# Optimization experiments

Measured on AMD Instinct MI355X. Metric: run time of the kernel, lower is better.

Reference implementation:

```python
import jax, jax.numpy as jnp
import numpy as np

D = 768
H = 12
DH = D // H
EPS = 1e-5

def _ln(x, g, b):
    m = jnp.mean(x, axis=-1, keepdims=True)
    v = jnp.mean(jnp.square(x - m), axis=-1, keepdims=True)
    return (x - m) * jax.lax.rsqrt(v + EPS) * g + b

def _gelu_new(x):
    c = jnp.float32(0.7978845608028654)  # sqrt(2/pi)
    return 0.5 * x * (1.0 + jnp.tanh(c * (x + 0.044715 * x * x * x)))

def setup_inputs() -> dict:
    key = jax.random.key(0)
    ks = jax.random.split(key, 12)
    s = lambda fan: 1.0 / np.sqrt(fan)
    return {
        "x": jax.random.normal(ks[0], (2, 1024, D), jnp.float32),
        "context_seq": jax.random.normal(ks[1], (2, 256, D), jnp.float32),
        "sos_h": jnp.zeros((D,), jnp.float32),
        "ln1_g": jnp.ones((D,), jnp.float32),
        "ln1_b": jnp.zeros((D,), jnp.float32),
        "W_attn": jax.random.normal(ks[2], (D, 3 * D), jnp.float32) * s(D),
        "b_attn": jnp.zeros((3 * D,), jnp.float32),
        "W_ref": jax.random.normal(ks[3], (D, 2 * D), jnp.float32) * s(D),
        "b_ref": jnp.zeros((2 * D,), jnp.float32),
        "W_proj": jax.random.normal(ks[4], (D, D), jnp.float32) * s(D),
        "b_proj": jnp.zeros((D,), jnp.float32),
        "ln2_g": jnp.ones((D,), jnp.float32),
        "ln2_b": jnp.zeros((D,), jnp.float32),
        "W_fc": jax.random.normal(ks[5], (D, 4 * D), jnp.float32) * s(D),
        "b_fc": jnp.zeros((4 * D,), jnp.float32),
        "W_mproj": jax.random.normal(ks[6], (4 * D, D), jnp.float32) * s(4 * D),
        "b_mproj": jnp.zeros((D,), jnp.float32),
    }

def _split_heads(t):  # [B,T,D] -> [B,H,T,dh]
    B, T, _ = t.shape
    return t.reshape(B, T, H, DH).transpose(0, 2, 1, 3)

def reference(x, context_seq, sos_h, ln1_g, ln1_b, W_attn, b_attn, W_ref, b_ref,
              W_proj, b_proj, ln2_g, ln2_b, W_fc, b_fc, W_mproj, b_mproj):
    B, S, _ = x.shape
    Sc = context_seq.shape[1]
    # prepend sos token (history_seq is None, history_seq_len = 0)
    sos = jnp.broadcast_to(sos_h.reshape(1, 1, D), (B, 1, D))
    h = jnp.concatenate([sos, x], axis=1)          # [B, S+1, D]
    hl = _ln(h, ln1_g, ln1_b)
    qkv = hl @ W_attn + b_attn
    q, k, v = jnp.split(qkv, 3, axis=-1)
    ckv = context_seq @ W_ref + b_ref
    kc, vc = jnp.split(ckv, 2, axis=-1)
    K = jnp.concatenate([kc, k], axis=1)            # [B, Sc+S+1, D]
    V = jnp.concatenate([vc, v], axis=1)
    qh, kh, vh = _split_heads(q), _split_heads(K), _split_heads(V)
    nd, ns = S + 1, Sc + S + 1
    w = jnp.einsum('bhqd,bhkd->bhqk', qh, kh) / jnp.float32(np.sqrt(DH))
    # causal bias window: query i attends to key j iff j <= i + Sc
    mask = jnp.arange(ns)[None, :] <= (jnp.arange(nd)[:, None] + Sc)
    w = jnp.where(mask[None, None], w, jnp.float32(-10000.0))
    w = jax.nn.softmax(w, axis=-1)
    a = jnp.einsum('bhqk,bhkd->bhqd', w, vh)        # [B,H,S+1,dh]
    a = a.transpose(0, 2, 1, 3).reshape(B, nd, D)
    a = a @ W_proj + b_proj
    h = h + a
    m = _gelu_new(_ln(h, ln2_g, ln2_b) @ W_fc + b_fc) @ W_mproj + b_mproj
    h = h + m
    return h[:, 1:, :]                               # drop sos position
```

## Files before the change

### kernel.cpp

```cpp
#include <hip/hip_runtime.h>
#include <math.h>

#define D0 768
#define NH 12
#define DHD 64
#define NB 2
#define SQ 1024
#define SCX 256
#define ND 1025
#define NS 1281
#define TT (NB*ND)
#define TP 2176
#define TC (NB*SCX)

typedef __attribute__((ext_vector_type(8))) short bf16x8;
typedef __attribute__((ext_vector_type(4))) float f32x4;

typedef const __attribute__((address_space(1))) unsigned int* gptr_t;
typedef __attribute__((address_space(3))) unsigned int* lptr_t;

__device__ __forceinline__ unsigned short f2bf(float f) {
    union { float f; unsigned u; } v; v.f = f;
    unsigned r = v.u + 0x7FFFu + ((v.u >> 16) & 1u);
    return (unsigned short)(r >> 16);
}

__device__ __forceinline__ float gelu_new(float x) {
    float x3 = x*x*x;
    float u = 0.7978845608028654f*(x + 0.044715f*x3);
    return 0.5f*x*(1.f + tanhf(u));
}

struct PrepArgs {
    const float* x; const float* sos; float* h;
    const float* ctx; unsigned short* ctxb;
    const float* W[5]; unsigned short* Wt[5];
    int K[5], N[5], nblk[5];
};

#define NBH 1538
#define NCVT 192

__global__ __launch_bounds__(256) void k_prep(PrepArgs a) {
    __shared__ float t[32][33];
    const int tid = threadIdx.x;
    int bid = blockIdx.x;
    if (bid < NBH) {
        int idx = bid*256 + tid;
        if (idx < TT*192) {
            int r = idx/192, c4 = idx%192;
            int b = r/ND, tt = r%ND;
            float4 v;
            if (tt == 0) v = ((const float4*)a.sos)[c4];
            else         v = ((const float4*)a.x)[(size_t)(b*SQ + tt - 1)*192 + c4];
            ((float4*)a.h)[(size_t)r*192 + c4] = v;
        }
        return;
    }
    bid -= NBH;
    if (bid < NCVT) {
        int i = bid*256 + tid;
        float4 p = ((const float4*)a.ctx)[i*2];
        float4 q = ((const float4*)a.ctx)[i*2+1];
        uint4 o;
        o.x = (unsigned)f2bf(p.x) | ((unsigned)f2bf(p.y) << 16);
        o.y = (unsigned)f2bf(p.z) | ((unsigned)f2bf(p.w) << 16);
        o.z = (unsigned)f2bf(q.x) | ((unsigned)f2bf(q.y) << 16);
        o.w = (unsigned)f2bf(q.z) | ((unsigned)f2bf(q.w) << 16);
        ((uint4*)a.ctxb)[i] = o;
        return;
    }
    bid -= NCVT;
    #pragma unroll
    for (int wi = 0; wi < 5; ++wi) {
        if (bid < a.nblk[wi]) {
            const float* W = a.W[wi];
            unsigned short* Wt = a.Wt[wi];
            const int K = a.K[wi], N = a.N[wi];
            const int nbx = N >> 5;
            const int n0 = (bid % nbx)*32, k0 = (bid / nbx)*32;
            const int r = tid >> 3, c4 = (tid & 7)*4;
            float4 v = *(const float4*)&W[(size_t)(k0+r)*N + n0 + c4];
            t[r][c4+0]=v.x; t[r][c4+1]=v.y; t[r][c4+2]=v.z; t[r][c4+3]=v.w;
            __syncthreads();
            ushort4 o;
            o.x = f2bf(t[c4+0][r]); o.y = f2bf(t[c4+1][r]);
            o.z = f2bf(t[c4+2][r]); o.w = f2bf(t[c4+3][r]);
            *(ushort4*)&Wt[(size_t)(n0+r)*K + k0 + c4] = o;
            return;
        }
        bid -= a.nblk[wi];
    }
}

__global__ __launch_bounds__(256) void k_ln(const float* __restrict__ in,
                                            const float* __restrict__ add,
                                            const float* __restrict__ g,
                                            const float* __restrict__ beta,
                                            unsigned short* __restrict__ out,
                                            float* __restrict__ resid,
                                            int nvalid) {
    int r = blockIdx.x;
    int tid = threadIdx.x;
    const size_t base = (size_t)r*D0;
    if (r >= nvalid) {
        out[base+tid] = 0; out[base+tid+256] = 0; out[base+tid+512] = 0;
        return;
    }
    float v0 = in[base+tid], v1 = in[base+tid+256], v2 = in[base+tid+512];
    if (add) {
        v0 += add[base+tid]; v1 += add[base+tid+256]; v2 += add[base+tid+512];
        resid[base+tid] = v0; resid[base+tid+256] = v1; resid[base+tid+512] = v2;
    }
    float s = v0+v1+v2;
    float ss = v0*v0 + v1*v1 + v2*v2;
    #pragma unroll
    for (int o = 32; o >= 1; o >>= 1) {
        s  += __shfl_down(s, o);
        ss += __shfl_down(ss, o);
    }
    __shared__ float red[8];
    __shared__ float mv[2];
    int w = tid >> 6;
    if ((tid & 63) == 0) { red[w] = s; red[4+w] = ss; }
    __syncthreads();
    if (tid == 0) {
        float S1 = red[0]+red[1]+red[2]+red[3];
        float S2 = red[4]+red[5]+red[6]+red[7];
        float mean = S1 * (1.f/D0);
        float var  = S2 * (1.f/D0) - mean*mean;
        mv[0] = mean; mv[1] = rsqrtf(var + 1e-5f);
    }
    __syncthreads();
    float mean = mv[0], rstd = mv[1];
    out[base+tid]     = f2bf((v0-mean)*rstd*g[tid]     + beta[tid]);
    out[base+tid+256] = f2bf((v1-mean)*rstd*g[tid+256] + beta[tid+256]);
    out[base+tid+512] = f2bf((v2-mean)*rstd*g[tid+512] + beta[tid+512]);
}

template<int GELU, int OUTBF>
__device__ __forceinline__ void gemm64_body(unsigned short* As, unsigned short* Bs,
                                            const unsigned short* __restrict__ A,
                                            const unsigned short* __restrict__ Bt,
                                            const float* __restrict__ bias,
                                            void* __restrict__ Cv,
                                            int N, int K, int bx, int by) {
    const int tid = threadIdx.x;
    const int w = tid >> 6;
    const int l = tid & 63;
    const int wm = w >> 1, wn = w & 1;
    const int m0 = by * 64, n0 = bx * 64;

    f32x4 acc[2][2] = {};

    for (int k0 = 0; k0 < K; k0 += 64) {
        __syncthreads();
        #pragma unroll
        for (int i = 0; i < 2; ++i) {
            int s = i*256 + tid;
            int row = s >> 3;
            int ch  = (s & 7) ^ (row & 7);
            const unsigned short* ga = A  + (size_t)(m0 + row)*K + k0 + ch*8;
            const unsigned short* gb = Bt + (size_t)(n0 + row)*K + k0 + ch*8;
            lptr_t la = (lptr_t)(As + (i*256 + w*64)*8);
            lptr_t lb = (lptr_t)(Bs + (i*256 + w*64)*8);
            __builtin_amdgcn_global_load_lds((gptr_t)ga, la, 16, 0, 0);
            __builtin_amdgcn_global_load_lds((gptr_t)gb, lb, 16, 0, 0);
        }
        __syncthreads();
        #pragma unroll
        for (int kc = 0; kc < 2; ++kc) {
            const int kchunk = kc*4 + (l >> 4);
            bf16x8 a[2], b[2];
            #pragma unroll
            for (int mi = 0; mi < 2; ++mi) {
                int row = wm*32 + mi*16 + (l & 15);
                a[mi] = *(const bf16x8*)&As[row*64 + ((kchunk ^ (row & 7))*8)];
            }
            #pragma unroll
            for (int ni = 0; ni < 2; ++ni) {
                int row = wn*32 + ni*16 + (l & 15);
                b[ni] = *(const bf16x8*)&Bs[row*64 + ((kchunk ^ (row & 7))*8)];
            }
            #pragma unroll
            for (int mi = 0; mi < 2; ++mi)
                #pragma unroll
                for (int ni = 0; ni < 2; ++ni)
                    acc[mi][ni] = __builtin_amdgcn_mfma_f32_16x16x32_bf16(a[mi], b[ni], acc[mi][ni], 0, 0, 0);
        }
    }

    float* Cf = (float*)Cv;
    unsigned short* Cb = (unsigned short*)Cv;
    const int rbase = m0 + wm*32 + (l >> 4)*4;
    const int cbase = n0 + wn*32 + (l & 15);
    #pragma unroll
    for (int ni = 0; ni < 2; ++ni) {
        int col = cbase + ni*16;
        float bv = bias[col];
        #pragma unroll
        for (int mi = 0; mi < 2; ++mi) {
            #pragma unroll
            for (int r = 0; r < 4; ++r) {
                int row = rbase + mi*16 + r;
                float v = acc[mi][ni][r] + bv;
                if (GELU) v = gelu_new(v);
                if (OUTBF) Cb[(size_t)row*N + col] = f2bf(v);
                else       Cf[(size_t)row*N + col] = v;
            }
        }
    }
}

template<int GELU, int OUTBF>
__global__ __launch_bounds__(256) void k_gemm64(const unsigned short* __restrict__ A,
                                                const unsigned short* __restrict__ Bt,
                                                const float* __restrict__ bias,
                                                void* __restrict__ Cv,
                                                int N, int K) {
    __shared__ unsigned short As[64*64];
    __shared__ unsigned short Bs[64*64];
    gemm64_body<GELU,OUTBF>(As, Bs, A, Bt, bias, Cv, N, K, blockIdx.x, blockIdx.y);
}

__global__ __launch_bounds__(256) void k_gemm_qkvckv(const unsigned short* __restrict__ hlb,
                                                     const unsigned short* __restrict__ WatT,
                                                     const float* __restrict__ bat,
                                                     unsigned short* __restrict__ qkvb,
                                                     const unsigned short* __restrict__ ctxb,
                                                     const unsigned short* __restrict__ WrefT,
                                                     const float* __restrict__ bref,
                                                     unsigned short* __restrict__ ckvb) {
    __shared__ unsigned short As[64*64];
    __shared__ unsigned short Bs[64*64];
    int bid = blockIdx.x;
    if (bid < (2304/64)*(TP/64)) {
        gemm64_body<0,1>(As, Bs, hlb, WatT, bat, qkvb, 2304, 768, bid % (2304/64), bid / (2304/64));
    } else {
        bid -= (2304/64)*(TP/64);
        gemm64_body<0,1>(As, Bs, ctxb, WrefT, bref, ckvb, 1536, 768, bid % (1536/64), bid / (1536/64));
    }
}

__global__ __launch_bounds__(256, 2) void k_attn_mfma(const unsigned short* __restrict__ qkvb,
                                                      const unsigned short* __restrict__ ckvb,
                                                      unsigned short* __restrict__ attnob) {
    const int bh = blockIdx.y;
    const int b = bh / NH, hh = bh % NH;
    const int tid = threadIdx.x;
    const int w = tid >> 6;
    const int l = tid & 63;
    const int lg = l >> 4;
    const int ll = l & 15;

    const int q0 = (16 - blockIdx.x) * 64;
    const int qw = q0 + w*16;

    __shared__ unsigned short Ks[64*64];
    __shared__ unsigned short Vt[64*64];
    __shared__ unsigned short Ps[4][16*64];

    bf16x8 qf[2];
    {
        int qc = min(qw + ll, ND-1);
        const unsigned short* qrow = qkvb + (size_t)(b*ND + qc)*2304 + hh*64;
        qf[0] = *(const bf16x8*)(qrow + lg*8);
        qf[1] = *(const bf16x8*)(qrow + 32 + lg*8);
    }

    f32x4 o_acc[4] = {};
    float mrow[4], lrow[4];
    #pragma unroll
    for (int i = 0; i < 4; ++i) { mrow[i] = -1e30f; lrow[i] = 0.f; }

    const int qmax_blk = min(q0 + 63, ND-1);
    const int ntiles = (qmax_blk + SCX)/64 + 1;
    const int klim_wave = qw + 15 + SCX;

    for (int kt = 0; kt < ntiles; ++kt) {
        __syncthreads();
        #pragma unroll
        for (int it = 0; it < 2; ++it) {
            int slot = it*256 + tid;
            int key  = slot >> 3;
            int ch   = (slot & 7) ^ (key & 7);
            int kg   = min(kt*64 + key, NS-1);
            const unsigned short* src;
            if (kg < SCX) src = ckvb + (size_t)(b*SCX + kg)*1536 + hh*64 + ch*8;
            else          src = qkvb + (size_t)(b*ND + kg - SCX)*2304 + 768 + hh*64 + ch*8;
            __builtin_amdgcn_global_load_lds((gptr_t)src, (lptr_t)(Ks + (size_t)(it*256 + w*64)*8), 16, 0, 0);
        }
        {
            int kv0 = (tid & 31)*2;
            int dch = tid >> 5;
            int kg0 = min(kt*64 + kv0,     NS-1);
            int kg1 = min(kt*64 + kv0 + 1, NS-1);
            const unsigned short* s0 = (kg0 < SCX)
                ? ckvb + (size_t)(b*SCX + kg0)*1536 + 768 + hh*64 + dch*8
                : qkvb + (size_t)(b*ND + kg0 - SCX)*2304 + 1536 + hh*64 + dch*8;
            const unsigned short* s1 = (kg1 < SCX)
                ? ckvb + (size_t)(b*SCX + kg1)*1536 + 768 + hh*64 + dch*8
                : qkvb + (size_t)(b*ND + kg1 - SCX)*2304 + 1536 + hh*64 + dch*8;
            union { uint4 u; unsigned short s[8]; } r0, r1;
            r0.u = *(const uint4*)s0;
            r1.u = *(const uint4*)s1;
            #pragma unroll
            for (int i = 0; i < 8; ++i) {
                int d = dch*8 + i;
                unsigned val = (unsigned)r0.s[i] | ((unsigned)r1.s[i] << 16);
                *(unsigned*)((char*)Vt + d*128 + (((kv0>>3) ^ (d&7))*16) + ((kv0&7)*2)) = val;
            }
        }
        __syncthreads();

        if (kt*64 > klim_wave) continue;

        bf16x8 kf[4][2];
        #pragma unroll
        for (int c = 0; c < 4; ++c) {
            int key = c*16 + ll;
            #pragma unroll
            for (int kc = 0; kc < 2; ++kc)
                kf[c][kc] = *(const bf16x8*)((char*)Ks + key*128 + (((kc*4 + lg) ^ (key&7))*16));
        }
        f32x4 s_acc[4];
        #pragma unroll
        for (int c = 0; c < 4; ++c) {
            f32x4 z = {0.f, 0.f, 0.f, 0.f};
            z = __builtin_amdgcn_mfma_f32_16x16x32_bf16(qf[0], kf[c][0], z, 0, 0, 0);
            s_acc[c] = __builtin_amdgcn_mfma_f32_16x16x32_bf16(qf[1], kf[c][1], z, 0, 0, 0);
        }

        const int kbase = kt*64;
        if (kbase + 63 > qw + SCX) {
            #pragma unroll
            for (int c = 0; c < 4; ++c) {
                int key = kbase + c*16 + ll;
                #pragma unroll
                for (int i = 0; i < 4; ++i) {
                    int q = qw + lg*4 + i;
                    if (key > q + SCX) s_acc[c][i] = -1e30f;
                }
            }
        }

        float tmax[4];
        #pragma unroll
        for (int i = 0; i < 4; ++i) {
            float tm = fmaxf(fmaxf(s_acc[0][i], s_acc[1][i]),
                             fmaxf(s_acc[2][i], s_acc[3][i]));
            #pragma unroll
            for (int o = 1; o < 16; o <<= 1) tm = fmaxf(tm, __shfl_xor(tm, o));
            tmax[i] = tm;
        }
        #pragma unroll
        for (int i = 0; i < 4; ++i) {
            float mnew = fmaxf(mrow[i], tmax[i]*0.125f);
            float fs = __expf(mrow[i] - mnew);
            mrow[i] = mnew;
            lrow[i] *= fs;
            #pragma unroll
            for (int dc = 0; dc < 4; ++dc) o_acc[dc][i] *= fs;
        }
        float psum[4] = {0.f, 0.f, 0.f, 0.f};
        #pragma unroll
        for (int c = 0; c < 4; ++c) {
            int kv = c*16 + ll;
            #pragma unroll
            for (int i = 0; i < 4; ++i) {
                float p = __expf(fmaf(s_acc[c][i], 0.125f, -mrow[i]));
                psum[i] += p;
                int q = lg*4 + i;
                union { float f; unsigned u; } cv; cv.f = p;
                *(unsigned short*)((char*)Ps[w] + q*128 + (((kv>>3) ^ (q&7))*16) + ((kv&7)*2))
                    = (unsigned short)((cv.u + 0x8000u) >> 16);
            }
        }
        #pragma unroll
        for (int i = 0; i < 4; ++i) {
            float s = psum[i];
            #pragma unroll
            for (int o = 1; o < 16; o <<= 1) s += __shfl_xor(s, o);
            lrow[i] += s;
        }

        #pragma unroll
        for (int kc = 0; kc < 2; ++kc) {
            int q = ll;
            bf16x8 pf = *(const bf16x8*)((char*)Ps[w] + q*128 + (((kc*4 + lg) ^ (q&7))*16));
            #pragma unroll
            for (int dc = 0; dc < 4; ++dc) {
                int d = dc*16 + ll;
                bf16x8 vf = *(const bf16x8*)((char*)Vt + d*128 + (((kc*4 + lg) ^ (d&7))*16));
                o_acc[dc] = __builtin_amdgcn_mfma_f32_16x16x32_bf16(pf, vf, o_acc[dc], 0, 0, 0);
            }
        }
    }

    #pragma unroll
    for (int i = 0; i < 4; ++i) {
        int q = qw + lg*4 + i;
        if (q >= ND) continue;
        float inv = 1.f / lrow[i];
        unsigned short* orow = attnob + (size_t)(b*ND + q)*768 + hh*64;
        #pragma unroll
        for (int dc = 0; dc < 4; ++dc)
            orow[dc*16 + ll] = f2bf(o_acc[dc][i] * inv);
    }
}

__global__ void k_final(const float* __restrict__ h, const float* __restrict__ mp,
                        float* __restrict__ out) {
    int idx = blockIdx.x*blockDim.x + threadIdx.x;
    const int total = NB*SQ*192;
    if (idx >= total) return;
    int r = idx/192, c4 = idx%192;
    int b = r/SQ, t = r%SQ;
    size_t hr = (size_t)(b*ND + t + 1)*192 + c4;
    float4 hv = ((const float4*)h)[hr];
    float4 mv = ((const float4*)mp)[hr];
    ((float4*)out)[idx] = make_float4(hv.x+mv.x, hv.y+mv.y, hv.z+mv.z, hv.w+mv.w);
}

extern "C" void kernel_launch(void* const* d_in, const int* in_sizes, int n_in,
                              void* d_out, int out_size, void* d_ws, size_t ws_size,
                              hipStream_t stream) {
    const float* x     = (const float*)d_in[0];
    const float* ctx   = (const float*)d_in[1];
    const float* sos   = (const float*)d_in[2];
    const float* ln1g  = (const float*)d_in[3];
    const float* ln1b  = (const float*)d_in[4];
    const float* Wat   = (const float*)d_in[5];
    const float* bat   = (const float*)d_in[6];
    const float* Wref  = (const float*)d_in[7];
    const float* bref  = (const float*)d_in[8];
    const float* Wpj   = (const float*)d_in[9];
    const float* bpj   = (const float*)d_in[10];
    const float* ln2g  = (const float*)d_in[11];
    const float* ln2b  = (const float*)d_in[12];
    const float* Wfc   = (const float*)d_in[13];
    const float* bfc   = (const float*)d_in[14];
    const float* Wmp   = (const float*)d_in[15];
    const float* bmp   = (const float*)d_in[16];
    float* out = (float*)d_out;

    char* p = (char*)d_ws;
    float* h      = (float*)p;  p += (size_t)TP*768*4;
    float* aproj  = (float*)p;  p += (size_t)TP*768*4;
    unsigned short* qkvb   = (unsigned short*)p;  p += (size_t)TP*2304*2;
    unsigned short* ckvb   = (unsigned short*)p;  p += (size_t)TC*1536*2;
    unsigned short* hlb    = (unsigned short*)p;  p += (size_t)TP*768*2;
    unsigned short* attnob = (unsigned short*)p;  p += (size_t)TP*768*2;
    unsigned short* mfcb   = (unsigned short*)p;  p += (size_t)TP*3072*2;
    unsigned short* ctxb   = (unsigned short*)p;  p += (size_t)TC*768*2;
    unsigned short* WatT   = (unsigned short*)p;  p += (size_t)2304*768*2;
    unsigned short* WrefT  = (unsigned short*)p;  p += (size_t)1536*768*2;
    unsigned short* WpjT   = (unsigned short*)p;  p += (size_t)768*768*2;
    unsigned short* WfcT   = (unsigned short*)p;  p += (size_t)3072*768*2;
    unsigned short* WmpT   = (unsigned short*)p;  p += (size_t)768*3072*2;

    PrepArgs pa;
    pa.x = x; pa.sos = sos; pa.h = h; pa.ctx = ctx; pa.ctxb = ctxb;
    pa.W[0]=Wat;  pa.Wt[0]=WatT;  pa.K[0]=768;  pa.N[0]=2304; pa.nblk[0]=(2304/32)*(768/32);
    pa.W[1]=Wref; pa.Wt[1]=WrefT; pa.K[1]=768;  pa.N[1]=1536; pa.nblk[1]=(1536/32)*(768/32);
    pa.W[2]=Wpj;  pa.Wt[2]=WpjT;  pa.K[2]=768;  pa.N[2]=768;  pa.nblk[2]=(768/32)*(768/32);
    pa.W[3]=Wfc;  pa.Wt[3]=WfcT;  pa.K[3]=768;  pa.N[3]=3072; pa.nblk[3]=(3072/32)*(768/32);
    pa.W[4]=Wmp;  pa.Wt[4]=WmpT;  pa.K[4]=3072; pa.N[4]=768;  pa.nblk[4]=(768/32)*(3072/32);
    int nprep = NBH + NCVT + pa.nblk[0]+pa.nblk[1]+pa.nblk[2]+pa.nblk[3]+pa.nblk[4];

    k_prep<<<dim3(nprep), dim3(256), 0, stream>>>(pa);
    k_ln<<<dim3(TP), dim3(256), 0, stream>>>(h, nullptr, ln1g, ln1b, hlb, nullptr, TT);
    k_gemm_qkvckv<<<dim3((2304/64)*(TP/64) + (1536/64)*(TC/64)), dim3(256), 0, stream>>>(
        hlb, WatT, bat, qkvb, ctxb, WrefT, bref, ckvb);
    k_attn_mfma<<<dim3(17, NB*NH), dim3(256), 0, stream>>>(qkvb, ckvb, attnob);
    k_gemm64<0,0><<<dim3(768/64, TP/64), dim3(256), 0, stream>>>(attnob, WpjT, bpj, aproj, 768, 768);
    k_ln<<<dim3(TP), dim3(256), 0, stream>>>(h, aproj, ln2g, ln2b, hlb, h, TT);
    k_gemm64<1,1><<<dim3(3072/64, TP/64), dim3(256), 0, stream>>>(hlb, WfcT, bfc, mfcb, 3072, 768);
    k_gemm64<0,0><<<dim3(768/64, TP/64), dim3(256), 0, stream>>>(mfcb, WmpT, bmp, aproj, 768, 3072);
    k_final<<<dim3((NB*SQ*192 + 255)/256), dim3(256), 0, stream>>>(h, aproj, out);
}
```

Baseline: 255.3 us.

## Double-buffer K/V tiles in attention kernel to overlap loads with compute

The attention kernel now keeps two LDS buffers each for K and transposed V. It issues the next tile's async K copy and V register loads before computing on the current tile, then writes V into the alternate buffer after compute. This aims to hide global-load latency behind the MFMA and softmax work, and it drops to one barrier per iteration. In exchange LDS use doubles and V stays live in registers across the compute, which could lower occupancy.

```diff
diff --git a/kernel.cpp b/kernel.cpp
--- a/kernel.cpp
+++ b/kernel.cpp
@@ -256,8 +256,8 @@
     const int q0 = (16 - blockIdx.x) * 64;
     const int qw = q0 + w*16;
 
-    __shared__ unsigned short Ks[64*64];
-    __shared__ unsigned short Vt[64*64];
+    __shared__ unsigned short Ks[2][64*64];
+    __shared__ unsigned short Vt[2][64*64];
     __shared__ unsigned short Ps[4][16*64];
 
     bf16x8 qf[2];
@@ -268,6 +268,9 @@
         qf[1] = *(const bf16x8*)(qrow + 32 + lg*8);
     }
 
+    const int kv0 = (tid & 31)*2;
+    const int dch = tid >> 5;
+
     f32x4 o_acc[4] = {};
     float mrow[4], lrow[4];
     #pragma unroll
@@ -277,124 +280,144 @@
     const int ntiles = (qmax_blk + SCX)/64 + 1;
     const int klim_wave = qw + 15 + SCX;
 
-    for (int kt = 0; kt < ntiles; ++kt) {
-        __syncthreads();
+    auto stageK = [&](int kt, int bb) {
         #pragma unroll
         for (int it = 0; it < 2; ++it) {
             int slot = it*256 + tid;
             int key  = slot >> 3;
             int ch   = (slot & 7) ^ (key & 7);
             int kg   = min(kt*64 + key, NS-1);
-            const unsigned short* src;
-            if (kg < SCX) src = ckvb + (size_t)(b*SCX + kg)*1536 + hh*64 + ch*8;
-            else          src = qkvb + (size_t)(b*ND + kg - SCX)*2304 + 768 + hh*64 + ch*8;
-            __builtin_amdgcn_global_load_lds((gptr_t)src, (lptr_t)(Ks + (size_t)(it*256 + w*64)*8), 16, 0, 0);
-        }
-        {
-            int kv0 = (tid & 31)*2;
-            int dch = tid >> 5;
-            int kg0 = min(kt*64 + kv0,     NS-1);
-            int kg1 = min(kt*64 + kv0 + 1, NS-1);
-            const unsigned short* s0 = (kg0 < SCX)
-                ? ckvb + (size_t)(b*SCX + kg0)*1536 + 768 + hh*64 + dch*8
-                : qkvb + (size_t)(b*ND + kg0 - SCX)*2304 + 1536 + hh*64 + dch*8;
-            const unsigned short* s1 = (kg1 < SCX)
-                ? ckvb + (size_t)(b*SCX + kg1)*1536 + 768 + hh*64 + dch*8
-                : qkvb + (size_t)(b*ND + kg1 - SCX)*2304 + 1536 + hh*64 + dch*8;
-            union { uint4 u; unsigned short s[8]; } r0, r1;
-            r0.u = *(const uint4*)s0;
-            r1.u = *(const uint4*)s1;
-            #pragma unroll
-            for (int i = 0; i < 8; ++i) {
-                int d = dch*8 + i;
-                unsigned val = (unsigned)r0.s[i] | ((unsigned)r1.s[i] << 16);
-                *(unsigned*)((char*)Vt + d*128 + (((kv0>>3) ^ (d&7))*16) + ((kv0&7)*2)) = val;
-            }
-        }
+            const unsigned short* src = (kg < SCX)
+                ? ckvb + (size_t)(b*SCX + kg)*1536 + hh*64 + ch*8
+                : qkvb + (size_t)(b*ND + kg - SCX)*2304 + 768 + hh*64 + ch*8;
+            __builtin_amdgcn_global_load_lds((gptr_t)src, (lptr_t)(Ks[bb] + (size_t)(it*256 + w*64)*8), 16, 0, 0);
+        }
+    };
+    auto loadV = [&](int kt, uint4& r0, uint4& r1) {
+        int kg0 = min(kt*64 + kv0,     NS-1);
+        int kg1 = min(kt*64 + kv0 + 1, NS-1);
+        const unsigned short* s0 = (kg0 < SCX)
+            ? ckvb + (size_t)(b*SCX + kg0)*1536 + 768 + hh*64 + dch*8
+            : qkvb + (size_t)(b*ND + kg0 - SCX)*2304 + 1536 + hh*64 + dch*8;
+        const unsigned short* s1 = (kg1 < SCX)
+            ? ckvb + (size_t)(b*SCX + kg1)*1536 + 768 + hh*64 + dch*8
+            : qkvb + (size_t)(b*ND + kg1 - SCX)*2304 + 1536 + hh*64 + dch*8;
+        r0 = *(const uint4*)s0;
+        r1 = *(const uint4*)s1;
+    };
+    auto writeV = [&](int bb, uint4 r0, uint4 r1) {
+        union { uint4 u; unsigned short s[8]; } u0, u1;
+        u0.u = r0; u1.u = r1;
+        #pragma unroll
+        for (int i = 0; i < 8; ++i) {
+            int d = dch*8 + i;
+            unsigned val = (unsigned)u0.s[i] | ((unsigned)u1.s[i] << 16);
+            *(unsigned*)((char*)Vt[bb] + d*128 + (((kv0>>3) ^ (d&7))*16) + ((kv0&7)*2)) = val;
+        }
+    };
+
+    stageK(0, 0);
+    { uint4 r0, r1; loadV(0, r0, r1); writeV(0, r0, r1); }
+    __syncthreads();
+
+    int cur = 0;
+    for (int kt = 0; kt < ntiles; ++kt) {
+        uint4 vr0, vr1;
+        const bool pre = (kt + 1 < ntiles);
+        if (pre) {
+            stageK(kt + 1, cur ^ 1);
+            loadV(kt + 1, vr0, vr1);
+        }
+
+        if (kt*64 <= klim_wave) {
+            const unsigned short* Kc = Ks[cur];
+            const unsigned short* Vc = Vt[cur];
+
+            bf16x8 kf[4][2];
+            #pragma unroll
+            for (int c = 0; c < 4; ++c) {
+                int key = c*16 + ll;
+                #pragma unroll
+                for (int kc = 0; kc < 2; ++kc)
+                    kf[c][kc] = *(const bf16x8*)((const char*)Kc + key*128 + (((kc*4 + lg) ^ (key&7))*16));
+            }
+            f32x4 s_acc[4];
+            #pragma unroll
+            for (int c = 0; c < 4; ++c) {
+                f32x4 z = {0.f, 0.f, 0.f, 0.f};
+                z = __builtin_amdgcn_mfma_f32_16x16x32_bf16(qf[0], kf[c][0], z, 0, 0, 0);
+                s_acc[c] = __builtin_amdgcn_mfma_f32_16x16x32_bf16(qf[1], kf[c][1], z, 0, 0, 0);
+            }
+
+            const int kbase = kt*64;
+            if (kbase + 63 > qw + SCX) {
+                #pragma unroll
+                for (int c = 0; c < 4; ++c) {
+                    int key = kbase + c*16 + ll;
+                    #pragma unroll
+                    for (int i = 0; i < 4; ++i) {
+                        int q = qw + lg*4 + i;
+                        if (key > q + SCX) s_acc[c][i] = -1e30f;
+                    }
+                }
+            }
+
+            float tmax[4];
+            #pragma unroll
+            for (int i = 0; i < 4; ++i) {
+                float tm = fmaxf(fmaxf(s_acc[0][i], s_acc[1][i]),
+                                 fmaxf(s_acc[2][i], s_acc[3][i]));
+                #pragma unroll
+                for (int o = 1; o < 16; o <<= 1) tm = fmaxf(tm, __shfl_xor(tm, o));
+                tmax[i] = tm;
+            }
+            #pragma unroll
+            for (int i = 0; i < 4; ++i) {
+                float mnew = fmaxf(mrow[i], tmax[i]*0.125f);
+                float fs = __expf(mrow[i] - mnew);
+                mrow[i] = mnew;
+                lrow[i] *= fs;
+                #pragma unroll
+                for (int dc = 0; dc < 4; ++dc) o_acc[dc][i] *= fs;
+            }
+            float psum[4] = {0.f, 0.f, 0.f, 0.f};
+            #pragma unroll
+            for (int c = 0; c < 4; ++c) {
+                int kv = c*16 + ll;
+                #pragma unroll
+                for (int i = 0; i < 4; ++i) {
+                    float p = __expf(fmaf(s_acc[c][i], 0.125f, -mrow[i]));
+                    psum[i] += p;
+                    int q = lg*4 + i;
+                    union { float f; unsigned u; } cv; cv.f = p;
+                    *(unsigned short*)((char*)Ps[w] + q*128 + (((kv>>3) ^ (q&7))*16) + ((kv&7)*2))
+                        = (unsigned short)((cv.u + 0x8000u) >> 16);
+                }
+            }
+            #pragma unroll
+            for (int i = 0; i < 4; ++i) {
+                float s = psum[i];
+                #pragma unroll
+                for (int o = 1; o < 16; o <<= 1) s += __shfl_xor(s, o);
+                lrow[i] += s;
+            }
+
+            #pragma unroll
+            for (int kc = 0; kc < 2; ++kc) {
+                int q = ll;
+                bf16x8 pf = *(const bf16x8*)((char*)Ps[w] + q*128 + (((kc*4 + lg) ^ (q&7))*16));
+                #pragma unroll
+                for (int dc = 0; dc < 4; ++dc) {
+                    int d = dc*16 + ll;
+                    bf16x8 vf = *(const bf16x8*)((const char*)Vc + d*128 + (((kc*4 + lg) ^ (d&7))*16));
+                    o_acc[dc] = __builtin_amdgcn_mfma_f32_16x16x32_bf16(pf, vf, o_acc[dc], 0, 0, 0);
+                }
+            }
+        }
+
+        if (pre) writeV(cur ^ 1, vr0, vr1);
         __syncthreads();
-
-        if (kt*64 > klim_wave) continue;
-
-        bf16x8 kf[4][2];
-        #pragma unroll
-        for (int c = 0; c < 4; ++c) {
-            int key = c*16 + ll;
-            #pragma unroll
-            for (int kc = 0; kc < 2; ++kc)
-                kf[c][kc] = *(const bf16x8*)((char*)Ks + key*128 + (((kc*4 + lg) ^ (key&7))*16));
-        }
-        f32x4 s_acc[4];
-        #pragma unroll
-        for (int c = 0; c < 4; ++c) {
-            f32x4 z = {0.f, 0.f, 0.f, 0.f};
-            z = __builtin_amdgcn_mfma_f32_16x16x32_bf16(qf[0], kf[c][0], z, 0, 0, 0);
-            s_acc[c] = __builtin_amdgcn_mfma_f32_16x16x32_bf16(qf[1], kf[c][1], z, 0, 0, 0);
-        }
-
-        const int kbase = kt*64;
-        if (kbase + 63 > qw + SCX) {
-            #pragma unroll
-            for (int c = 0; c < 4; ++c) {
-                int key = kbase + c*16 + ll;
-                #pragma unroll
-                for (int i = 0; i < 4; ++i) {
-                    int q = qw + lg*4 + i;
-                    if (key > q + SCX) s_acc[c][i] = -1e30f;
-                }
-            }
-        }
-
-        float tmax[4];
-        #pragma unroll
-        for (int i = 0; i < 4; ++i) {
-            float tm = fmaxf(fmaxf(s_acc[0][i], s_acc[1][i]),
-                             fmaxf(s_acc[2][i], s_acc[3][i]));
-            #pragma unroll
-            for (int o = 1; o < 16; o <<= 1) tm = fmaxf(tm, __shfl_xor(tm, o));
-            tmax[i] = tm;
-        }
-        #pragma unroll
-        for (int i = 0; i < 4; ++i) {
-            float mnew = fmaxf(mrow[i], tmax[i]*0.125f);
-            float fs = __expf(mrow[i] - mnew);
-            mrow[i] = mnew;
-            lrow[i] *= fs;
-            #pragma unroll
-            for (int dc = 0; dc < 4; ++dc) o_acc[dc][i] *= fs;
-        }
-        float psum[4] = {0.f, 0.f, 0.f, 0.f};
-        #pragma unroll
-        for (int c = 0; c < 4; ++c) {
-            int kv = c*16 + ll;
-            #pragma unroll
-            for (int i = 0; i < 4; ++i) {
-                float p = __expf(fmaf(s_acc[c][i], 0.125f, -mrow[i]));
-                psum[i] += p;
-                int q = lg*4 + i;
-                union { float f; unsigned u; } cv; cv.f = p;
-                *(unsigned short*)((char*)Ps[w] + q*128 + (((kv>>3) ^ (q&7))*16) + ((kv&7)*2))
-                    = (unsigned short)((cv.u + 0x8000u) >> 16);
-            }
-        }
-        #pragma unroll
-        for (int i = 0; i < 4; ++i) {
-            float s = psum[i];
-            #pragma unroll
-            for (int o = 1; o < 16; o <<= 1) s += __shfl_xor(s, o);
-            lrow[i] += s;
-        }
-
-        #pragma unroll
-        for (int kc = 0; kc < 2; ++kc) {
-            int q = ll;
-            bf16x8 pf = *(const bf16x8*)((char*)Ps[w] + q*128 + (((kc*4 + lg) ^ (q&7))*16));
-            #pragma unroll
-            for (int dc = 0; dc < 4; ++dc) {
-                int d = dc*16 + ll;
-                bf16x8 vf = *(const bf16x8*)((char*)Vt + d*128 + (((kc*4 + lg) ^ (d&7))*16));
-                o_acc[dc] = __builtin_amdgcn_mfma_f32_16x16x32_bf16(pf, vf, o_acc[dc], 0, 0, 0);
-            }
-        }
+        cur ^= 1;
     }
 
     #pragma unroll
```

Result: slower. 263.1 us (+3.1%).

## Split attention keys across waves with per-wave tiles and LDS merge

Applied to the files above, without the earlier changes.

The attention kernel now gives each block 16 query rows instead of 64. The four waves split the key range in interleaved 32-key tiles, and each wave loads its own K/V tiles into private LDS, so the per-tile __syncthreads go away. The partial softmax states (max, sum, output) of the four waves are merged through LDS at the end in a flash-decoding style reduction. This raises the grid from 17 to 65 query blocks per head and the occupancy hint to 4 blocks per CU, aiming for better parallelism and load balance. The cost is more K/V reloading from global memory across blocks and an extra final merge pass.

```diff
diff --git a/kernel.cpp b/kernel.cpp
--- a/kernel.cpp
+++ b/kernel.cpp
@@ -242,7 +242,7 @@
     }
 }
 
-__global__ __launch_bounds__(256, 2) void k_attn_mfma(const unsigned short* __restrict__ qkvb,
+__global__ __launch_bounds__(256, 4) void k_attn_mfma(const unsigned short* __restrict__ qkvb,
                                                       const unsigned short* __restrict__ ckvb,
                                                       unsigned short* __restrict__ attnob) {
     const int bh = blockIdx.y;
@@ -253,16 +253,16 @@
     const int lg = l >> 4;
     const int ll = l & 15;
 
-    const int q0 = (16 - blockIdx.x) * 64;
-    const int qw = q0 + w*16;
-
-    __shared__ unsigned short Ks[64*64];
-    __shared__ unsigned short Vt[64*64];
-    __shared__ unsigned short Ps[4][16*64];
+    const int q0 = (64 - blockIdx.x) * 16;
+
+    __shared__ unsigned short lds_u16[18432];
+    unsigned short* Kw = lds_u16 + w*4608;
+    unsigned short* Vw = Kw + 2048;
+    unsigned short* Pw = Kw + 4096;
 
     bf16x8 qf[2];
     {
-        int qc = min(qw + ll, ND-1);
+        int qc = min(q0 + ll, ND-1);
         const unsigned short* qrow = qkvb + (size_t)(b*ND + qc)*2304 + hh*64;
         qf[0] = *(const bf16x8*)(qrow + lg*8);
         qf[1] = *(const bf16x8*)(qrow + 32 + lg*8);
@@ -273,28 +273,27 @@
     #pragma unroll
     for (int i = 0; i < 4; ++i) { mrow[i] = -1e30f; lrow[i] = 0.f; }
 
-    const int qmax_blk = min(q0 + 63, ND-1);
-    const int ntiles = (qmax_blk + SCX)/64 + 1;
-    const int klim_wave = qw + 15 + SCX;
-
-    for (int kt = 0; kt < ntiles; ++kt) {
-        __syncthreads();
-        #pragma unroll
-        for (int it = 0; it < 2; ++it) {
-            int slot = it*256 + tid;
+    const int klim = min(q0 + 15 + SCX, NS-1);
+
+    for (int kt = w; kt*32 <= klim; kt += 4) {
+        #pragma unroll
+        for (int it = 0; it < 4; ++it) {
+            int slot = it*64 + l;
             int key  = slot >> 3;
             int ch   = (slot & 7) ^ (key & 7);
-            int kg   = min(kt*64 + key, NS-1);
-            const unsigned short* src;
-            if (kg < SCX) src = ckvb + (size_t)(b*SCX + kg)*1536 + hh*64 + ch*8;
-            else          src = qkvb + (size_t)(b*ND + kg - SCX)*2304 + 768 + hh*64 + ch*8;
-            __builtin_amdgcn_global_load_lds((gptr_t)src, (lptr_t)(Ks + (size_t)(it*256 + w*64)*8), 16, 0, 0);
-        }
-        {
-            int kv0 = (tid & 31)*2;
-            int dch = tid >> 5;
-            int kg0 = min(kt*64 + kv0,     NS-1);
-            int kg1 = min(kt*64 + kv0 + 1, NS-1);
+            int kg   = min(kt*32 + key, NS-1);
+            const unsigned short* src = (kg < SCX)
+                ? ckvb + (size_t)(b*SCX + kg)*1536 + hh*64 + ch*8
+                : qkvb + (size_t)(b*ND + kg - SCX)*2304 + 768 + hh*64 + ch*8;
+            __builtin_amdgcn_global_load_lds((gptr_t)src, (lptr_t)(Kw + it*512), 16, 0, 0);
+        }
+        #pragma unroll
+        for (int it = 0; it < 2; ++it) {
+            int kp  = l & 15;
+            int dch = (l >> 4) + it*4;
+            int kv0 = kp*2;
+            int kg0 = min(kt*32 + kv0,     NS-1);
+            int kg1 = min(kt*32 + kv0 + 1, NS-1);
             const unsigned short* s0 = (kg0 < SCX)
                 ? ckvb + (size_t)(b*SCX + kg0)*1536 + 768 + hh*64 + dch*8
                 : qkvb + (size_t)(b*ND + kg0 - SCX)*2304 + 1536 + hh*64 + dch*8;
@@ -305,40 +304,39 @@
             r0.u = *(const uint4*)s0;
             r1.u = *(const uint4*)s1;
             #pragma unroll
-            for (int i = 0; i < 8; ++i) {
-                int d = dch*8 + i;
-                unsigned val = (unsigned)r0.s[i] | ((unsigned)r1.s[i] << 16);
-                *(unsigned*)((char*)Vt + d*128 + (((kv0>>3) ^ (d&7))*16) + ((kv0&7)*2)) = val;
-            }
-        }
-        __syncthreads();
-
-        if (kt*64 > klim_wave) continue;
-
-        bf16x8 kf[4][2];
-        #pragma unroll
-        for (int c = 0; c < 4; ++c) {
+            for (int j = 0; j < 8; ++j) {
+                int d = dch*8 + j;
+                unsigned val = (unsigned)r0.s[j] | ((unsigned)r1.s[j] << 16);
+                *(unsigned*)(Vw + d*32 + (((kp>>2) ^ ((d>>2)&3))*8) + (kp&3)*2) = val;
+            }
+        }
+        asm volatile("s_waitcnt vmcnt(0) lgkmcnt(0)" ::: "memory");
+        __builtin_amdgcn_sched_barrier(0);
+
+        bf16x8 kf[2][2];
+        #pragma unroll
+        for (int c = 0; c < 2; ++c) {
             int key = c*16 + ll;
             #pragma unroll
             for (int kc = 0; kc < 2; ++kc)
-                kf[c][kc] = *(const bf16x8*)((char*)Ks + key*128 + (((kc*4 + lg) ^ (key&7))*16));
-        }
-        f32x4 s_acc[4];
-        #pragma unroll
-        for (int c = 0; c < 4; ++c) {
+                kf[c][kc] = *(const bf16x8*)(Kw + key*64 + (((kc*4 + lg) ^ (key&7))*8));
+        }
+        f32x4 s_acc[2];
+        #pragma unroll
+        for (int c = 0; c < 2; ++c) {
             f32x4 z = {0.f, 0.f, 0.f, 0.f};
             z = __builtin_amdgcn_mfma_f32_16x16x32_bf16(qf[0], kf[c][0], z, 0, 0, 0);
             s_acc[c] = __builtin_amdgcn_mfma_f32_16x16x32_bf16(qf[1], kf[c][1], z, 0, 0, 0);
         }
 
-        const int kbase = kt*64;
-        if (kbase + 63 > qw + SCX) {
-            #pragma unroll
-            for (int c = 0; c < 4; ++c) {
+        const int kbase = kt*32;
+        if (kbase + 31 > q0 + SCX) {
+            #pragma unroll
+            for (int c = 0; c < 2; ++c) {
                 int key = kbase + c*16 + ll;
                 #pragma unroll
                 for (int i = 0; i < 4; ++i) {
-                    int q = qw + lg*4 + i;
+                    int q = q0 + lg*4 + i;
                     if (key > q + SCX) s_acc[c][i] = -1e30f;
                 }
             }
@@ -347,8 +345,7 @@
         float tmax[4];
         #pragma unroll
         for (int i = 0; i < 4; ++i) {
-            float tm = fmaxf(fmaxf(s_acc[0][i], s_acc[1][i]),
-                             fmaxf(s_acc[2][i], s_acc[3][i]));
+            float tm = fmaxf(s_acc[0][i], s_acc[1][i]);
             #pragma unroll
             for (int o = 1; o < 16; o <<= 1) tm = fmaxf(tm, __shfl_xor(tm, o));
             tmax[i] = tm;
@@ -364,7 +361,7 @@
         }
         float psum[4] = {0.f, 0.f, 0.f, 0.f};
         #pragma unroll
-        for (int c = 0; c < 4; ++c) {
+        for (int c = 0; c < 2; ++c) {
             int kv = c*16 + ll;
             #pragma unroll
             for (int i = 0; i < 4; ++i) {
@@ -372,7 +369,7 @@
                 psum[i] += p;
                 int q = lg*4 + i;
                 union { float f; unsigned u; } cv; cv.f = p;
-                *(unsigned short*)((char*)Ps[w] + q*128 + (((kv>>3) ^ (q&7))*16) + ((kv&7)*2))
+                Pw[q*32 + (((kv>>3) ^ ((q>>2)&3))*8) + (kv&7)]
                     = (unsigned short)((cv.u + 0x8000u) >> 16);
             }
         }
@@ -384,28 +381,53 @@
             lrow[i] += s;
         }
 
-        #pragma unroll
-        for (int kc = 0; kc < 2; ++kc) {
-            int q = ll;
-            bf16x8 pf = *(const bf16x8*)((char*)Ps[w] + q*128 + (((kc*4 + lg) ^ (q&7))*16));
-            #pragma unroll
-            for (int dc = 0; dc < 4; ++dc) {
-                int d = dc*16 + ll;
-                bf16x8 vf = *(const bf16x8*)((char*)Vt + d*128 + (((kc*4 + lg) ^ (d&7))*16));
-                o_acc[dc] = __builtin_amdgcn_mfma_f32_16x16x32_bf16(pf, vf, o_acc[dc], 0, 0, 0);
-            }
-        }
-    }
-
+        bf16x8 pf = *(const bf16x8*)(Pw + ll*32 + ((lg ^ ((ll>>2)&3))*8));
+        #pragma unroll
+        for (int dc = 0; dc < 4; ++dc) {
+            int d = dc*16 + ll;
+            bf16x8 vf = *(const bf16x8*)(Vw + d*32 + ((lg ^ ((d>>2)&3))*8));
+            o_acc[dc] = __builtin_amdgcn_mfma_f32_16x16x32_bf16(pf, vf, o_acc[dc], 0, 0, 0);
+        }
+    }
+
+    __syncthreads();
+    {
+        float* Om = (float*)(lds_u16 + w*2176);
+        float* ml = (float*)(lds_u16 + 8704 + w*64);
+        #pragma unroll
+        for (int dc = 0; dc < 4; ++dc)
+            #pragma unroll
+            for (int i = 0; i < 4; ++i)
+                Om[(lg*4 + i)*68 + dc*16 + ll] = o_acc[dc][i];
+        if (ll == 0) {
+            #pragma unroll
+            for (int i = 0; i < 4; ++i) {
+                ml[(lg*4 + i)*2]     = mrow[i];
+                ml[(lg*4 + i)*2 + 1] = lrow[i];
+            }
+        }
+    }
+    __syncthreads();
     #pragma unroll
     for (int i = 0; i < 4; ++i) {
-        int q = qw + lg*4 + i;
-        if (q >= ND) continue;
-        float inv = 1.f / lrow[i];
-        unsigned short* orow = attnob + (size_t)(b*ND + q)*768 + hh*64;
-        #pragma unroll
-        for (int dc = 0; dc < 4; ++dc)
-            orow[dc*16 + ll] = f2bf(o_acc[dc][i] * inv);
+        int row = lg*4 + i;
+        float mw[4], lw[4];
+        #pragma unroll
+        for (int wp = 0; wp < 4; ++wp) {
+            const float* mlp = (const float*)(lds_u16 + 8704 + wp*64);
+            mw[wp] = mlp[row*2]; lw[wp] = mlp[row*2 + 1];
+        }
+        float M = fmaxf(fmaxf(mw[0], mw[1]), fmaxf(mw[2], mw[3]));
+        float L = 0.f, acc = 0.f;
+        #pragma unroll
+        for (int wp = 0; wp < 4; ++wp) {
+            float sc = __expf(mw[wp] - M);
+            L += lw[wp]*sc;
+            acc += sc * ((const float*)(lds_u16 + wp*2176))[row*68 + w*16 + ll];
+        }
+        int q = q0 + row;
+        if (q < ND)
+            attnob[(size_t)(b*ND + q)*768 + hh*64 + w*16 + ll] = f2bf(acc / L);
     }
 }
 
@@ -472,7 +494,7 @@
     k_ln<<<dim3(TP), dim3(256), 0, stream>>>(h, nullptr, ln1g, ln1b, hlb, nullptr, TT);
     k_gemm_qkvckv<<<dim3((2304/64)*(TP/64) + (1536/64)*(TC/64)), dim3(256), 0, stream>>>(
         hlb, WatT, bat, qkvb, ctxb, WrefT, bref, ckvb);
-    k_attn_mfma<<<dim3(17, NB*NH), dim3(256), 0, stream>>>(qkvb, ckvb, attnob);
+    k_attn_mfma<<<dim3(65, NB*NH), dim3(256), 0, stream>>>(qkvb, ckvb, attnob);
     k_gemm64<0,0><<<dim3(768/64, TP/64), dim3(256), 0, stream>>>(attnob, WpjT, bpj, aproj, 768, 768);
     k_ln<<<dim3(TP), dim3(256), 0, stream>>>(h, aproj, ln2g, ln2b, hlb, h, TT);
     k_gemm64<1,1><<<dim3(3072/64, TP/64), dim3(256), 0, stream>>>(hlb, WfcT, bfc, mfcb, 3072, 768);
```

After: 263.6 us. 1.03x slower.
